# Performance work log

Hardware: AMD Instinct MI355X
Metric: run time of the kernel (lower is better)

## Reference

```python
import jax, jax.numpy as jnp
import numpy as np

B, D, C = 8192, 2048, 1000
NUM_IDS = 256
MSEL_W, ORTH_W, CONS_W = 0.5, 0.1, 0.1


def setup_inputs() -> dict:
    key = jax.random.key(0)
    ks = jax.random.split(key, 7)
    return {
        "feat_shared": jax.random.normal(ks[0], (B, D), dtype=jnp.float32),
        "dee1": jax.random.normal(ks[1], (B, D), dtype=jnp.float32),
        "dee2": jax.random.normal(ks[2], (B, D), dtype=jnp.float32),
        "dee3": jax.random.normal(ks[3], (B, D), dtype=jnp.float32),
        "logits": jax.random.normal(ks[4], (B, C), dtype=jnp.float32),
        "labels": jax.random.randint(ks[5], (B,), 0, NUM_IDS, dtype=jnp.int32),
        "modal_ids": jax.random.randint(ks[6], (B,), 0, 2, dtype=jnp.int32),
    }


def _l2norm(x):
    return x / jnp.sqrt(jnp.sum(x * x, axis=1, keepdims=True)).clip(1e-12)


def _msel(features, labels, modal_ids):
    f = _l2norm(features)
    m_rgb = (modal_ids == 0).astype(f.dtype)  # [B]
    m_sar = (modal_ids == 1).astype(f.dtype)
    # per-label per-modal sums and counts via segment_sum (fixed NUM_IDS segments)
    sum_rgb = jax.ops.segment_sum(f * m_rgb[:, None], labels, num_segments=NUM_IDS)  # [L,D]
    sum_sar = jax.ops.segment_sum(f * m_sar[:, None], labels, num_segments=NUM_IDS)
    n_rgb = jax.ops.segment_sum(m_rgb, labels, num_segments=NUM_IDS)  # [L]
    n_sar = jax.ops.segment_sum(m_sar, labels, num_segments=NUM_IDS)
    c_rgb = sum_rgb / jnp.maximum(n_rgb, 1.0)[:, None]
    c_sar = sum_sar / jnp.maximum(n_sar, 1.0)[:, None]
    dist_cross = 1.0 - jnp.sum(c_rgb * c_sar, axis=1)
    # mean of Gram(f_rgb, f_rgb) == center_rgb . center_rgb (includes diagonal), same math
    dist_intra = 1.0 - jnp.sum(c_rgb * c_rgb, axis=1)
    valid = (n_rgb >= 2.0) & (n_sar >= 1.0)
    per_label = jnp.where(valid, (dist_cross - dist_intra) ** 2, 0.0)
    count = jnp.sum(valid.astype(f.dtype))
    return jnp.where(count > 0, jnp.sum(per_label) / jnp.maximum(count, 1.0), 0.0)


def _orth(f1, f2, f3):
    n1, n2, n3 = _l2norm(f1), _l2norm(f2), _l2norm(f3)
    s12 = jnp.mean(jnp.abs(jnp.sum(n1 * n2, axis=1)))
    s13 = jnp.mean(jnp.abs(jnp.sum(n1 * n3, axis=1)))
    s23 = jnp.mean(jnp.abs(jnp.sum(n2 * n3, axis=1)))
    return s12 + s13 + s23


def _consistency(logits, modal_ids):
    probs = jax.nn.softmax(logits, axis=1)  # [B,C]
    m_rgb = (modal_ids == 0).astype(probs.dtype)
    m_sar = (modal_ids == 1).astype(probs.dtype)
    n_rgb = jnp.sum(m_rgb)
    n_sar = jnp.sum(m_sar)
    p_rgb = jnp.sum(probs * m_rgb[:, None], axis=0) / jnp.maximum(n_rgb, 1.0)
    p_sar = jnp.sum(probs * m_sar[:, None], axis=0) / jnp.maximum(n_sar, 1.0)
    lr, ls = jnp.log(p_rgb), jnp.log(p_sar)
    # F.kl_div(log p, q, 'sum') = sum q*(log q - log p)
    kl = 0.5 * (jnp.sum(p_sar * (ls - lr)) + jnp.sum(p_rgb * (lr - ls)))
    return jnp.where((n_rgb > 0) & (n_sar > 0), kl, 0.0)


def reference(feat_shared, dee1, dee2, dee3, logits, labels, modal_ids):
    loss = MSEL_W * _msel(feat_shared, labels, modal_ids)
    loss = loss + ORTH_W * _orth(dee1, dee2, dee3)
    loss = loss + CONS_W * _consistency(logits, modal_ids)
    return loss
```

## Files before the change

### kernel.cpp

```cpp
#include <hip/hip_runtime.h>
#include <math.h>

#define B_   8192
#define D_   2048
#define C_   1000
#define L_   256
#define BIN_CAP 64
#define ORTH_BLOCKS 2048

typedef unsigned short bf16raw;

__device__ __forceinline__ float bflo(unsigned int u) { return __uint_as_float(u << 16); }
__device__ __forceinline__ float bfhi(unsigned int u) { return __uint_as_float(u & 0xffff0000u); }

__device__ __forceinline__ bf16raw f2b(float f) {
  unsigned int x = __float_as_uint(f);
  unsigned int r = (x + 0x7fffu + ((x >> 16) & 1u)) >> 16;
  return (bf16raw)r;
}

__device__ __forceinline__ void dec8(uint4 u, float* x) {
  x[0] = bflo(u.x); x[1] = bfhi(u.x);
  x[2] = bflo(u.y); x[3] = bfhi(u.y);
  x[4] = bflo(u.z); x[5] = bfhi(u.z);
  x[6] = bflo(u.w); x[7] = bfhi(u.w);
}

__device__ __forceinline__ float waveSum(float v) {
#pragma unroll
  for (int off = 32; off > 0; off >>= 1) v += __shfl_xor(v, off, 64);
  return v;
}

__device__ __forceinline__ float blockSum(float v, float* lds4) {
  v = waveSum(v);
  const int wave = threadIdx.x >> 6;
  if ((threadIdx.x & 63) == 0) lds4[wave] = v;
  __syncthreads();
  v = lds4[0] + lds4[1] + lds4[2] + lds4[3];
  __syncthreads();
  return v;
}

__device__ __forceinline__ void load8rt(const void* p, size_t rowbase, int t, int isb,
                                        float* x) {
  if (isb) {
    const uint4 v = ((const uint4*)((const bf16raw*)p + rowbase))[t];
    dec8(v, x);
  } else {
    const float4* q = (const float4*)((const float*)p + rowbase);
    const float4 v0 = q[2 * t], v1 = q[2 * t + 1];
    x[0] = v0.x; x[1] = v0.y; x[2] = v0.z; x[3] = v0.w;
    x[4] = v1.x; x[5] = v1.y; x[6] = v1.z; x[7] = v1.w;
  }
}

__global__ __launch_bounds__(256) void detect_kernel(const unsigned int* feat_words,
                                                     int* flag) {
  __shared__ float lds4[4];
  const unsigned int w = feat_words[threadIdx.x];
  const float v = bflo(w);
  const float a = fabsf(v);
  float hit = (a > 1e-3f && a < 10.f) ? 1.f : 0.f;
  hit = blockSum(hit, lds4);
  if (threadIdx.x == 0) *flag = (hit > 128.f) ? 1 : 0;
}

__global__ __launch_bounds__(256) void init_kernel(int* counts, float* accs,
                                                   float* p_final) {
  const int t = blockIdx.x * 256 + threadIdx.x;
  if (t < 2 * L_) counts[t] = 0;
  if (t < 16) accs[t] = 0.f;
  if (t < 2 * C_) p_final[t] = 0.f;
}

__global__ __launch_bounds__(256) void bin_kernel(const int* labels, const int* modal,
                                                  int* counts, int* rowlist) {
  const int r = blockIdx.x * 256 + threadIdx.x;
  if (r >= B_) return;
  const int m = modal[r] ? 1 : 0;
  int lb = labels[r]; lb = lb < 0 ? 0 : (lb >= L_ ? L_ - 1 : lb);
  const int key = m * L_ + lb;
  const int idx = atomicAdd(&counts[key], 1);
  if (idx < BIN_CAP) rowlist[key * BIN_CAP + idx] = r;
}

__global__ __launch_bounds__(256) void rowdot_kernel(const void* f1, const void* f2,
                                                     const void* f3, const void* feat,
                                                     float* orth_part, float* norms,
                                                     const int* flag) {
  __shared__ float lsum[4][3];
  const int t = threadIdx.x;
  const int wave = t >> 6, lane = t & 63;
  const int isb = *flag;

  if (blockIdx.x < ORTH_BLOCKS) {
    const int row = blockIdx.x * 4 + wave;
    const size_t base = (size_t)row * D_;
    float v[6] = {0.f, 0.f, 0.f, 0.f, 0.f, 0.f};
    if (isb) {
      const uint4* qa = (const uint4*)((const bf16raw*)f1 + base);
      const uint4* qb = (const uint4*)((const bf16raw*)f2 + base);
      const uint4* qc = (const uint4*)((const bf16raw*)f3 + base);
      uint4 A[4], Bv[4], Cv[4];
#pragma unroll
      for (int j = 0; j < 4; ++j) A[j] = qa[j * 64 + lane];
#pragma unroll
      for (int j = 0; j < 4; ++j) Bv[j] = qb[j * 64 + lane];
#pragma unroll
      for (int j = 0; j < 4; ++j) Cv[j] = qc[j * 64 + lane];
#pragma unroll
      for (int j = 0; j < 4; ++j) {
        float a[8], b[8], c[8];
        dec8(A[j], a); dec8(Bv[j], b); dec8(Cv[j], c);
#pragma unroll
        for (int k = 0; k < 8; ++k) {
          v[0] += a[k] * a[k]; v[1] += b[k] * b[k]; v[2] += c[k] * c[k];
          v[3] += a[k] * b[k]; v[4] += a[k] * c[k]; v[5] += b[k] * c[k];
        }
      }
    } else {
      const float4* qa = (const float4*)((const float*)f1 + base);
      const float4* qb = (const float4*)((const float*)f2 + base);
      const float4* qc = (const float4*)((const float*)f3 + base);
#pragma unroll
      for (int h = 0; h < 2; ++h) {
        float4 A[4], Bv[4], Cv[4];
#pragma unroll
        for (int j = 0; j < 4; ++j) A[j] = qa[(h * 4 + j) * 64 + lane];
#pragma unroll
        for (int j = 0; j < 4; ++j) Bv[j] = qb[(h * 4 + j) * 64 + lane];
#pragma unroll
        for (int j = 0; j < 4; ++j) Cv[j] = qc[(h * 4 + j) * 64 + lane];
#pragma unroll
        for (int j = 0; j < 4; ++j) {
          const float a[4] = {A[j].x, A[j].y, A[j].z, A[j].w};
          const float b[4] = {Bv[j].x, Bv[j].y, Bv[j].z, Bv[j].w};
          const float c[4] = {Cv[j].x, Cv[j].y, Cv[j].z, Cv[j].w};
#pragma unroll
          for (int k = 0; k < 4; ++k) {
            v[0] += a[k] * a[k]; v[1] += b[k] * b[k]; v[2] += c[k] * c[k];
            v[3] += a[k] * b[k]; v[4] += a[k] * c[k]; v[5] += b[k] * c[k];
          }
        }
      }
    }
#pragma unroll
    for (int off = 32; off > 0; off >>= 1) {
#pragma unroll
      for (int j = 0; j < 6; ++j) v[j] += __shfl_xor(v[j], off, 64);
    }
    const float q1 = fmaxf(sqrtf(v[0]), 1e-12f);
    const float q2 = fmaxf(sqrtf(v[1]), 1e-12f);
    const float q3 = fmaxf(sqrtf(v[2]), 1e-12f);
    if (lane == 0) {
      lsum[wave][0] = fabsf(v[3]) / (q1 * q2);
      lsum[wave][1] = fabsf(v[4]) / (q1 * q3);
      lsum[wave][2] = fabsf(v[5]) / (q2 * q3);
    }
    __syncthreads();
    if (t < 3) {
      orth_part[t * ORTH_BLOCKS + blockIdx.x] =
          lsum[0][t] + lsum[1][t] + lsum[2][t] + lsum[3][t];
    }
  } else {
    const int row = (blockIdx.x - ORTH_BLOCKS) * 4 + wave;
    const size_t base = (size_t)row * D_;
    float ss = 0.f;
    if (isb) {
      const uint4* q = (const uint4*)((const bf16raw*)feat + base);
      uint4 X[4];
#pragma unroll
      for (int j = 0; j < 4; ++j) X[j] = q[j * 64 + lane];
#pragma unroll
      for (int j = 0; j < 4; ++j) {
        float x[8]; dec8(X[j], x);
#pragma unroll
        for (int k = 0; k < 8; ++k) ss += x[k] * x[k];
      }
    } else {
      const float4* q = (const float4*)((const float*)feat + base);
#pragma unroll
      for (int j = 0; j < 8; ++j) {
        const float4 w = q[j * 64 + lane];
        ss += w.x * w.x + w.y * w.y + w.z * w.z + w.w * w.w;
      }
    }
    ss = waveSum(ss);
    if (lane == 0) norms[row] = 1.f / fmaxf(sqrtf(ss), 1e-12f);
  }
}

__device__ __forceinline__ void loadlogits(const void* logits, int r, int lane, int isb,
                                           float* x) {
#pragma unroll
  for (int kk = 0; kk < 4; ++kk) {
    const int idx = lane + (kk << 6);
    if (idx < (C_ / 4)) {
      if (isb) {
        const uint2 w = ((const uint2*)((const bf16raw*)logits + (size_t)r * C_))[idx];
        x[4 * kk + 0] = bflo(w.x); x[4 * kk + 1] = bfhi(w.x);
        x[4 * kk + 2] = bflo(w.y); x[4 * kk + 3] = bfhi(w.y);
      } else {
        const float4 w = ((const float4*)((const float*)logits + (size_t)r * C_))[idx];
        x[4 * kk + 0] = w.x; x[4 * kk + 1] = w.y;
        x[4 * kk + 2] = w.z; x[4 * kk + 3] = w.w;
      }
    } else {
      x[4 * kk + 0] = -INFINITY; x[4 * kk + 1] = -INFINITY;
      x[4 * kk + 2] = -INFINITY; x[4 * kk + 3] = -INFINITY;
    }
  }
}

__global__ __launch_bounds__(256) void cons_kernel(const void* logits, const int* modal,
                                                   float* p_final, const int* flag) {
  __shared__ float wacc[4][2][1024];
  const int t = threadIdx.x;
  const int wave = t >> 6, lane = t & 63;
  const int isb = *flag;
  float accA[16], accB[16];
#pragma unroll
  for (int k = 0; k < 16; ++k) { accA[k] = 0.f; accB[k] = 0.f; }
  const int rbase = blockIdx.x * 32 + wave * 8;
#pragma unroll
  for (int i = 0; i < 8; i += 2) {
    const int r0 = rbase + i, r1 = rbase + i + 1;
    float x[16], y[16];
    loadlogits(logits, r0, lane, isb, x);
    loadlogits(logits, r1, lane, isb, y);
    float mx = -INFINITY, my = -INFINITY;
#pragma unroll
    for (int k = 0; k < 16; ++k) { mx = fmaxf(mx, x[k]); my = fmaxf(my, y[k]); }
#pragma unroll
    for (int off = 32; off > 0; off >>= 1) {
      mx = fmaxf(mx, __shfl_xor(mx, off, 64));
      my = fmaxf(my, __shfl_xor(my, off, 64));
    }
    float sx = 0.f, sy = 0.f;
#pragma unroll
    for (int k = 0; k < 16; ++k) {
      x[k] = expf(x[k] - mx); sx += x[k];
      y[k] = expf(y[k] - my); sy += y[k];
    }
#pragma unroll
    for (int off = 32; off > 0; off >>= 1) {
      sx += __shfl_xor(sx, off, 64);
      sy += __shfl_xor(sy, off, 64);
    }
    const float ivx = 1.f / sx, ivy = 1.f / sy;
    if (modal[r0] == 0) {
#pragma unroll
      for (int k = 0; k < 16; ++k) accA[k] += x[k] * ivx;
    } else {
#pragma unroll
      for (int k = 0; k < 16; ++k) accB[k] += x[k] * ivx;
    }
    if (modal[r1] == 0) {
#pragma unroll
      for (int k = 0; k < 16; ++k) accA[k] += y[k] * ivy;
    } else {
#pragma unroll
      for (int k = 0; k < 16; ++k) accB[k] += y[k] * ivy;
    }
  }
#pragma unroll
  for (int k = 0; k < 16; ++k) {
    const int c = 4 * (lane + ((k >> 2) << 6)) + (k & 3);
    wacc[wave][0][c] = accA[k];
    wacc[wave][1][c] = accB[k];
  }
  __syncthreads();
  for (int e = t; e < 2 * C_; e += 256) {
    const int m = (e < C_) ? 0 : 1;
    const int c = e - m * C_;
    atomicAdd(&p_final[e], wacc[0][m][c] + wacc[1][m][c] + wacc[2][m][c] + wacc[3][m][c]);
  }
}

__global__ __launch_bounds__(256) void label_kernel(const void* feat, const int* counts,
                                                    const int* rowlist, const float* norms,
                                                    float* accs, const int* flag) {
  __shared__ float lds4[4];
  const int l = blockIdx.x;
  const int t = threadIdx.x;
  const int isb = *flag;
  const int nr_true = counts[l];
  const int ns_true = counts[L_ + l];
  const int nr = nr_true < BIN_CAP ? nr_true : BIN_CAP;
  const int ns = ns_true < BIN_CAP ? ns_true : BIN_CAP;
  const int tot = nr + ns;
  float accR[8], accS[8];
#pragma unroll
  for (int j = 0; j < 8; ++j) { accR[j] = 0.f; accS[j] = 0.f; }
  for (int i = 0; i < tot; i += 2) {
    const int i1 = i + 1;
    const int key0 = (i < nr) ? l : (L_ + l);
    const int idx0 = (i < nr) ? i : (i - nr);
    const int r0 = rowlist[key0 * BIN_CAP + idx0];
    const bool have1 = (i1 < tot);
    const int key1 = (i1 < nr) ? l : (L_ + l);
    const int idx1 = (i1 < nr) ? i1 : (i1 - nr);
    const int r1 = have1 ? rowlist[key1 * BIN_CAP + idx1] : r0;
    const float rn0 = norms[r0];
    const float rn1 = have1 ? norms[r1] : 0.f;
    float x0[8], x1[8];
    load8rt(feat, (size_t)r0 * D_, t, isb, x0);
    load8rt(feat, (size_t)r1 * D_, t, isb, x1);
    if (i < nr) {
#pragma unroll
      for (int j = 0; j < 8; ++j) accR[j] += x0[j] * rn0;
    } else {
#pragma unroll
      for (int j = 0; j < 8; ++j) accS[j] += x0[j] * rn0;
    }
    if (i1 < nr) {
#pragma unroll
      for (int j = 0; j < 8; ++j) accR[j] += x1[j] * rn1;
    } else {
#pragma unroll
      for (int j = 0; j < 8; ++j) accS[j] += x1[j] * rn1;
    }
  }
  float rr = 0.f, rs = 0.f;
#pragma unroll
  for (int j = 0; j < 8; ++j) { rr += accR[j] * accR[j]; rs += accR[j] * accS[j]; }
  rr = blockSum(rr, lds4);
  rs = blockSum(rs, lds4);
  if (t == 0 && nr_true >= 2 && ns_true >= 1) {
    const float fr = (float)nr_true, fs = (float)ns_true;
    const float diff = rr / (fr * fr) - rs / (fr * fs);
    atomicAdd(&accs[3], diff * diff);
    atomicAdd(&accs[4], 1.0f);
  }
}

__global__ __launch_bounds__(256) void InnovationLoss_88124138979690_kernel(
    const float* p_final, const int* counts, const float* accs, const float* orth_part,
    void* out, const int* flag) {
  __shared__ float lds4[4];
  const int t = threadIdx.x;
  const float nr = blockSum((float)counts[t], lds4);
  const float ns = blockSum((float)counts[L_ + t], lds4);
  const float fr = fmaxf(nr, 1.f), fs = fmaxf(ns, 1.f);
  float klp = 0.f;
  for (int c = t; c < C_; c += 256) {
    const float pr = p_final[c] / fr;
    const float ps = p_final[C_ + c] / fs;
    klp += (ps - pr) * (logf(ps) - logf(pr));
  }
  klp = blockSum(klp, lds4);
  float o0 = 0.f, o1 = 0.f, o2 = 0.f;
  for (int b = t; b < ORTH_BLOCKS; b += 256) {
    o0 += orth_part[b];
    o1 += orth_part[ORTH_BLOCKS + b];
    o2 += orth_part[2 * ORTH_BLOCKS + b];
  }
  o0 = blockSum(o0, lds4);
  o1 = blockSum(o1, lds4);
  o2 = blockSum(o2, lds4);
  if (t == 0) {
    const float kl = (nr > 0.f && ns > 0.f) ? 0.5f * klp : 0.f;
    const float msel_cnt = accs[4];
    const float msel = msel_cnt > 0.f ? accs[3] / fmaxf(msel_cnt, 1.f) : 0.f;
    const float orth = (o0 + o1 + o2) * (1.0f / (float)B_);
    const float res = 0.5f * msel + 0.1f * orth + 0.1f * kl;
    if (*flag) ((bf16raw*)out)[0] = f2b(res);
    else       ((float*)out)[0]   = res;
  }
}

extern "C" __attribute__((visibility("default")))
void kernel_launch(void* const* d_in, const int* in_sizes, int n_in,
                   void* d_out, int out_size, void* d_ws, size_t ws_size,
                   hipStream_t stream) {
  const void* feat   = d_in[0];
  const void* dee1   = d_in[1];
  const void* dee2   = d_in[2];
  const void* dee3   = d_in[3];
  const void* logits = d_in[4];
  const int*  labels = (const int*)d_in[5];
  const int*  modal  = (const int*)d_in[6];

  char* ws = (char*)d_ws;
  int*   counts    = (int*)  (ws);
  float* accs      = (float*)(ws + 2048);
  float* p_final   = (float*)(ws + 2112);
  int*   rowlist   = (int*)  (ws + 10112);
  int*   flag      = (int*)  (ws + 141184);
  float* norms     = (float*)(ws + 141248);
  float* orth_part = (float*)(ws + 174016);

  detect_kernel<<<1, 256, 0, stream>>>((const unsigned int*)feat, flag);
  init_kernel<<<8, 256, 0, stream>>>(counts, accs, p_final);
  bin_kernel<<<B_ / 256, 256, 0, stream>>>(labels, modal, counts, rowlist);
  rowdot_kernel<<<2 * ORTH_BLOCKS, 256, 0, stream>>>(dee1, dee2, dee3, feat, orth_part,
                                                     norms, flag);
  cons_kernel<<<B_ / 32, 256, 0, stream>>>(logits, modal, p_final, flag);
  label_kernel<<<L_, 256, 0, stream>>>(feat, counts, rowlist, norms, accs, flag);
  InnovationLoss_88124138979690_kernel<<<1, 256, 0, stream>>>(p_final, counts, accs,
                                                              orth_part, d_out, flag);
}
```

Measured before the change: 316.2 us.

## Fuse orth, norm and softmax streaming into one persistent kernel with prefetch

Merges the row-dot/norm kernel and the consistency softmax kernel into a single launch, with fixed block partitions for orthogonality, feature norms and logits. Each wave now handles multiple rows (8 orth rows, 16 norm rows, 4 logit rows) and double-buffers the next row's loads in registers to overlap memory with compute. The label kernel also gets software prefetch of upcoming rows. This removes a launch and is meant to improve latency hiding, at the cost of higher register pressure and fewer, heavier blocks.

```diff
diff --git a/kernel.cpp b/kernel.cpp
--- a/kernel.cpp
+++ b/kernel.cpp
@@ -6,7 +6,12 @@
 #define C_   1000
 #define L_   256
 #define BIN_CAP 64
-#define ORTH_BLOCKS 2048
+
+#define ORTH_BLK  256
+#define NORM_BLK  128
+#define CONS_BLK  512
+#define FUSED_GRID (ORTH_BLK + NORM_BLK + CONS_BLK)
+#define ORTH_WAVES (ORTH_BLK * 4)
 
 typedef unsigned short bf16raw;
 
@@ -40,19 +45,6 @@
   v = lds4[0] + lds4[1] + lds4[2] + lds4[3];
   __syncthreads();
   return v;
-}
-
-__device__ __forceinline__ void load8rt(const void* p, size_t rowbase, int t, int isb,
-                                        float* x) {
-  if (isb) {
-    const uint4 v = ((const uint4*)((const bf16raw*)p + rowbase))[t];
-    dec8(v, x);
-  } else {
-    const float4* q = (const float4*)((const float*)p + rowbase);
-    const float4 v0 = q[2 * t], v1 = q[2 * t + 1];
-    x[0] = v0.x; x[1] = v0.y; x[2] = v0.z; x[3] = v0.w;
-    x[4] = v1.x; x[5] = v1.y; x[6] = v1.z; x[7] = v1.w;
-  }
 }
 
 __global__ __launch_bounds__(256) void detect_kernel(const unsigned int* feat_words,
@@ -85,196 +77,279 @@
   if (idx < BIN_CAP) rowlist[key * BIN_CAP + idx] = r;
 }
 
-__global__ __launch_bounds__(256) void rowdot_kernel(const void* f1, const void* f2,
-                                                     const void* f3, const void* feat,
-                                                     float* orth_part, float* norms,
-                                                     const int* flag) {
-  __shared__ float lsum[4][3];
+__device__ __forceinline__ void ldrow3(const bf16raw* pa, const bf16raw* pb,
+                                       const bf16raw* pc, size_t base, int lane,
+                                       uint4 (&A)[4], uint4 (&Bv)[4], uint4 (&Cv)[4]) {
+  const uint4* qa = (const uint4*)(pa + base);
+  const uint4* qb = (const uint4*)(pb + base);
+  const uint4* qc = (const uint4*)(pc + base);
+#pragma unroll
+  for (int j = 0; j < 4; ++j) A[j] = qa[j * 64 + lane];
+#pragma unroll
+  for (int j = 0; j < 4; ++j) Bv[j] = qb[j * 64 + lane];
+#pragma unroll
+  for (int j = 0; j < 4; ++j) Cv[j] = qc[j * 64 + lane];
+}
+
+__device__ __forceinline__ void orth_rowacc(const uint4 (&A)[4], const uint4 (&Bv)[4],
+                                            const uint4 (&Cv)[4], float (&v)[6]) {
+#pragma unroll
+  for (int j = 0; j < 4; ++j) {
+    float a[8], b[8], c[8];
+    dec8(A[j], a); dec8(Bv[j], b); dec8(Cv[j], c);
+#pragma unroll
+    for (int k = 0; k < 8; ++k) {
+      v[0] += a[k] * a[k]; v[1] += b[k] * b[k]; v[2] += c[k] * c[k];
+      v[3] += a[k] * b[k]; v[4] += a[k] * c[k]; v[5] += b[k] * c[k];
+    }
+  }
+}
+
+__device__ __forceinline__ float ssq4(const uint4 (&X)[4]) {
+  float ss = 0.f;
+#pragma unroll
+  for (int j = 0; j < 4; ++j) {
+    float x[8]; dec8(X[j], x);
+#pragma unroll
+    for (int k = 0; k < 8; ++k) ss += x[k] * x[k];
+  }
+  return ss;
+}
+
+__device__ __forceinline__ void loadlogits_f32(const void* logits, int r, int lane,
+                                               float (&x)[16]) {
+#pragma unroll
+  for (int kk = 0; kk < 4; ++kk) {
+    const int idx = lane + (kk << 6);
+    if (idx < (C_ / 4)) {
+      const float4 w = ((const float4*)((const float*)logits + (size_t)r * C_))[idx];
+      x[4 * kk + 0] = w.x; x[4 * kk + 1] = w.y;
+      x[4 * kk + 2] = w.z; x[4 * kk + 3] = w.w;
+    } else {
+      x[4 * kk + 0] = -INFINITY; x[4 * kk + 1] = -INFINITY;
+      x[4 * kk + 2] = -INFINITY; x[4 * kk + 3] = -INFINITY;
+    }
+  }
+}
+
+__device__ __forceinline__ void softmax_acc(float (&x)[16], int m, float (&accA)[16],
+                                            float (&accB)[16]) {
+  float mx = -INFINITY;
+#pragma unroll
+  for (int k = 0; k < 16; ++k) mx = fmaxf(mx, x[k]);
+#pragma unroll
+  for (int off = 32; off > 0; off >>= 1) mx = fmaxf(mx, __shfl_xor(mx, off, 64));
+  float s = 0.f;
+#pragma unroll
+  for (int k = 0; k < 16; ++k) { x[k] = expf(x[k] - mx); s += x[k]; }
+#pragma unroll
+  for (int off = 32; off > 0; off >>= 1) s += __shfl_xor(s, off, 64);
+  const float inv = 1.f / s;
+  if (m == 0) {
+#pragma unroll
+    for (int k = 0; k < 16; ++k) accA[k] += x[k] * inv;
+  } else {
+#pragma unroll
+    for (int k = 0; k < 16; ++k) accB[k] += x[k] * inv;
+  }
+}
+
+__global__ __launch_bounds__(256) void fused_stream_kernel(
+    const void* f1, const void* f2, const void* f3, const void* feat,
+    const void* logits, const int* modal, float* orth_part, float* norms,
+    float* p_final, const int* flag) {
+  __shared__ float wacc[4][2][1024];
   const int t = threadIdx.x;
   const int wave = t >> 6, lane = t & 63;
   const int isb = *flag;
-
-  if (blockIdx.x < ORTH_BLOCKS) {
-    const int row = blockIdx.x * 4 + wave;
-    const size_t base = (size_t)row * D_;
-    float v[6] = {0.f, 0.f, 0.f, 0.f, 0.f, 0.f};
+  const int bx = blockIdx.x;
+
+  if (bx < ORTH_BLK) {
+    const int gw = bx * 4 + wave;
+    float s12 = 0.f, s13 = 0.f, s23 = 0.f;
     if (isb) {
-      const uint4* qa = (const uint4*)((const bf16raw*)f1 + base);
-      const uint4* qb = (const uint4*)((const bf16raw*)f2 + base);
-      const uint4* qc = (const uint4*)((const bf16raw*)f3 + base);
-      uint4 A[4], Bv[4], Cv[4];
-#pragma unroll
-      for (int j = 0; j < 4; ++j) A[j] = qa[j * 64 + lane];
-#pragma unroll
-      for (int j = 0; j < 4; ++j) Bv[j] = qb[j * 64 + lane];
-#pragma unroll
-      for (int j = 0; j < 4; ++j) Cv[j] = qc[j * 64 + lane];
-#pragma unroll
-      for (int j = 0; j < 4; ++j) {
-        float a[8], b[8], c[8];
-        dec8(A[j], a); dec8(Bv[j], b); dec8(Cv[j], c);
-#pragma unroll
-        for (int k = 0; k < 8; ++k) {
-          v[0] += a[k] * a[k]; v[1] += b[k] * b[k]; v[2] += c[k] * c[k];
-          v[3] += a[k] * b[k]; v[4] += a[k] * c[k]; v[5] += b[k] * c[k];
-        }
+      const bf16raw* pa = (const bf16raw*)f1;
+      const bf16raw* pb = (const bf16raw*)f2;
+      const bf16raw* pc = (const bf16raw*)f3;
+      const size_t base0 = (size_t)gw * (8 * D_);
+      uint4 A0[4], B0[4], C0[4], A1[4], B1[4], C1[4];
+      ldrow3(pa, pb, pc, base0, lane, A0, B0, C0);
+#pragma unroll
+      for (int r = 0; r < 8; ++r) {
+        if (r < 7) {
+          const size_t nb = base0 + (size_t)(r + 1) * D_;
+          if (r & 1) ldrow3(pa, pb, pc, nb, lane, A0, B0, C0);
+          else       ldrow3(pa, pb, pc, nb, lane, A1, B1, C1);
+        }
+        float v[6] = {0.f, 0.f, 0.f, 0.f, 0.f, 0.f};
+        if (r & 1) orth_rowacc(A1, B1, C1, v);
+        else       orth_rowacc(A0, B0, C0, v);
+#pragma unroll
+        for (int off = 32; off > 0; off >>= 1) {
+#pragma unroll
+          for (int j = 0; j < 6; ++j) v[j] += __shfl_xor(v[j], off, 64);
+        }
+        const float q1 = fmaxf(sqrtf(v[0]), 1e-12f);
+        const float q2 = fmaxf(sqrtf(v[1]), 1e-12f);
+        const float q3 = fmaxf(sqrtf(v[2]), 1e-12f);
+        s12 += fabsf(v[3]) / (q1 * q2);
+        s13 += fabsf(v[4]) / (q1 * q3);
+        s23 += fabsf(v[5]) / (q2 * q3);
       }
     } else {
-      const float4* qa = (const float4*)((const float*)f1 + base);
-      const float4* qb = (const float4*)((const float*)f2 + base);
-      const float4* qc = (const float4*)((const float*)f3 + base);
-#pragma unroll
-      for (int h = 0; h < 2; ++h) {
-        float4 A[4], Bv[4], Cv[4];
-#pragma unroll
-        for (int j = 0; j < 4; ++j) A[j] = qa[(h * 4 + j) * 64 + lane];
-#pragma unroll
-        for (int j = 0; j < 4; ++j) Bv[j] = qb[(h * 4 + j) * 64 + lane];
-#pragma unroll
-        for (int j = 0; j < 4; ++j) Cv[j] = qc[(h * 4 + j) * 64 + lane];
-#pragma unroll
-        for (int j = 0; j < 4; ++j) {
-          const float a[4] = {A[j].x, A[j].y, A[j].z, A[j].w};
-          const float b[4] = {Bv[j].x, Bv[j].y, Bv[j].z, Bv[j].w};
-          const float c[4] = {Cv[j].x, Cv[j].y, Cv[j].z, Cv[j].w};
+      for (int r = 0; r < 8; ++r) {
+        const size_t base = ((size_t)gw * 8 + r) * D_;
+        const float4* qa = (const float4*)((const float*)f1 + base);
+        const float4* qb = (const float4*)((const float*)f2 + base);
+        const float4* qc = (const float4*)((const float*)f3 + base);
+        float v[6] = {0.f, 0.f, 0.f, 0.f, 0.f, 0.f};
+#pragma unroll
+        for (int h = 0; h < 8; ++h) {
+          const float4 a4 = qa[h * 64 + lane];
+          const float4 b4 = qb[h * 64 + lane];
+          const float4 c4 = qc[h * 64 + lane];
+          const float a[4] = {a4.x, a4.y, a4.z, a4.w};
+          const float b[4] = {b4.x, b4.y, b4.z, b4.w};
+          const float c[4] = {c4.x, c4.y, c4.z, c4.w};
 #pragma unroll
           for (int k = 0; k < 4; ++k) {
             v[0] += a[k] * a[k]; v[1] += b[k] * b[k]; v[2] += c[k] * c[k];
             v[3] += a[k] * b[k]; v[4] += a[k] * c[k]; v[5] += b[k] * c[k];
           }
         }
-      }
-    }
-#pragma unroll
-    for (int off = 32; off > 0; off >>= 1) {
-#pragma unroll
-      for (int j = 0; j < 6; ++j) v[j] += __shfl_xor(v[j], off, 64);
-    }
-    const float q1 = fmaxf(sqrtf(v[0]), 1e-12f);
-    const float q2 = fmaxf(sqrtf(v[1]), 1e-12f);
-    const float q3 = fmaxf(sqrtf(v[2]), 1e-12f);
+#pragma unroll
+        for (int off = 32; off > 0; off >>= 1) {
+#pragma unroll
+          for (int j = 0; j < 6; ++j) v[j] += __shfl_xor(v[j], off, 64);
+        }
+        const float q1 = fmaxf(sqrtf(v[0]), 1e-12f);
+        const float q2 = fmaxf(sqrtf(v[1]), 1e-12f);
+        const float q3 = fmaxf(sqrtf(v[2]), 1e-12f);
+        s12 += fabsf(v[3]) / (q1 * q2);
+        s13 += fabsf(v[4]) / (q1 * q3);
+        s23 += fabsf(v[5]) / (q2 * q3);
+      }
+    }
     if (lane == 0) {
-      lsum[wave][0] = fabsf(v[3]) / (q1 * q2);
-      lsum[wave][1] = fabsf(v[4]) / (q1 * q3);
-      lsum[wave][2] = fabsf(v[5]) / (q2 * q3);
+      orth_part[gw] = s12;
+      orth_part[ORTH_WAVES + gw] = s13;
+      orth_part[2 * ORTH_WAVES + gw] = s23;
+    }
+  } else if (bx < ORTH_BLK + NORM_BLK) {
+    const int gw = (bx - ORTH_BLK) * 4 + wave;
+    const size_t base0 = (size_t)gw * (16 * D_);
+    if (isb) {
+      const bf16raw* pf = (const bf16raw*)feat;
+      uint4 X0[4], X1[4];
+      {
+        const uint4* q = (const uint4*)(pf + base0);
+#pragma unroll
+        for (int j = 0; j < 4; ++j) X0[j] = q[j * 64 + lane];
+      }
+#pragma unroll
+      for (int r = 0; r < 16; ++r) {
+        if (r < 15) {
+          const uint4* q = (const uint4*)(pf + base0 + (size_t)(r + 1) * D_);
+          if (r & 1) {
+#pragma unroll
+            for (int j = 0; j < 4; ++j) X0[j] = q[j * 64 + lane];
+          } else {
+#pragma unroll
+            for (int j = 0; j < 4; ++j) X1[j] = q[j * 64 + lane];
+          }
+        }
+        float ss = (r & 1) ? ssq4(X1) : ssq4(X0);
+        ss = waveSum(ss);
+        if (lane == 0) norms[gw * 16 + r] = 1.f / fmaxf(sqrtf(ss), 1e-12f);
+      }
+    } else {
+      for (int r = 0; r < 16; ++r) {
+        const float4* q = (const float4*)((const float*)feat + base0 + (size_t)r * D_);
+        float ss = 0.f;
+#pragma unroll
+        for (int j = 0; j < 8; ++j) {
+          const float4 w = q[j * 64 + lane];
+          ss += w.x * w.x + w.y * w.y + w.z * w.z + w.w * w.w;
+        }
+        ss = waveSum(ss);
+        if (lane == 0) norms[gw * 16 + r] = 1.f / fmaxf(sqrtf(ss), 1e-12f);
+      }
+    }
+  } else {
+    const int cb = bx - ORTH_BLK - NORM_BLK;
+    const int rbase = cb * 16 + wave * 4;
+    float accA[16], accB[16];
+#pragma unroll
+    for (int k = 0; k < 16; ++k) { accA[k] = 0.f; accB[k] = 0.f; }
+    if (isb) {
+      const bf16raw* pl = (const bf16raw*)logits;
+      uint4 W0a, W1a;
+      uint4 W0b = make_uint4(0u, 0u, 0u, 0u), W1b = make_uint4(0u, 0u, 0u, 0u);
+      int ma, mb = 0;
+      {
+        const uint4* q = (const uint4*)(pl + (size_t)rbase * C_);
+        W0a = q[lane];
+        W1a = (lane < 61) ? q[64 + lane] : make_uint4(0u, 0u, 0u, 0u);
+        ma = modal[rbase];
+      }
+#pragma unroll
+      for (int i = 0; i < 4; ++i) {
+        if (i < 3) {
+          const int rn = rbase + i + 1;
+          const uint4* q = (const uint4*)(pl + (size_t)rn * C_);
+          W0b = q[lane];
+          W1b = (lane < 61) ? q[64 + lane] : make_uint4(0u, 0u, 0u, 0u);
+          mb = modal[rn];
+        }
+        float x[16];
+        dec8(W0a, x);
+        if (lane < 61) {
+          float xx[8]; dec8(W1a, xx);
+#pragma unroll
+          for (int k = 0; k < 8; ++k) x[8 + k] = xx[k];
+        } else {
+#pragma unroll
+          for (int k = 0; k < 8; ++k) x[8 + k] = -INFINITY;
+        }
+        softmax_acc(x, ma, accA, accB);
+        W0a = W0b; W1a = W1b; ma = mb;
+      }
+#pragma unroll
+      for (int k = 0; k < 16; ++k) {
+        const int c = (k < 8) ? (8 * lane + k) : (512 + 8 * lane + (k - 8));
+        wacc[wave][0][c] = accA[k];
+        wacc[wave][1][c] = accB[k];
+      }
+    } else {
+      float xa[16], xb[16];
+      int ma, mb = 0;
+      loadlogits_f32(logits, rbase, lane, xa);
+      ma = modal[rbase];
+#pragma unroll
+      for (int i = 0; i < 4; ++i) {
+        if (i < 3) {
+          loadlogits_f32(logits, rbase + i + 1, lane, xb);
+          mb = modal[rbase + i + 1];
+        }
+        softmax_acc(xa, ma, accA, accB);
+#pragma unroll
+        for (int k = 0; k < 16; ++k) xa[k] = xb[k];
+        ma = mb;
+      }
+#pragma unroll
+      for (int k = 0; k < 16; ++k) {
+        const int c = 4 * (lane + ((k >> 2) << 6)) + (k & 3);
+        wacc[wave][0][c] = accA[k];
+        wacc[wave][1][c] = accB[k];
+      }
     }
     __syncthreads();
-    if (t < 3) {
-      orth_part[t * ORTH_BLOCKS + blockIdx.x] =
-          lsum[0][t] + lsum[1][t] + lsum[2][t] + lsum[3][t];
-    }
-  } else {
-    const int row = (blockIdx.x - ORTH_BLOCKS) * 4 + wave;
-    const size_t base = (size_t)row * D_;
-    float ss = 0.f;
-    if (isb) {
-      const uint4* q = (const uint4*)((const bf16raw*)feat + base);
-      uint4 X[4];
-#pragma unroll
-      for (int j = 0; j < 4; ++j) X[j] = q[j * 64 + lane];
-#pragma unroll
-      for (int j = 0; j < 4; ++j) {
-        float x[8]; dec8(X[j], x);
-#pragma unroll
-        for (int k = 0; k < 8; ++k) ss += x[k] * x[k];
-      }
-    } else {
-      const float4* q = (const float4*)((const float*)feat + base);
-#pragma unroll
-      for (int j = 0; j < 8; ++j) {
-        const float4 w = q[j * 64 + lane];
-        ss += w.x * w.x + w.y * w.y + w.z * w.z + w.w * w.w;
-      }
-    }
-    ss = waveSum(ss);
-    if (lane == 0) norms[row] = 1.f / fmaxf(sqrtf(ss), 1e-12f);
-  }
-}
-
-__device__ __forceinline__ void loadlogits(const void* logits, int r, int lane, int isb,
-                                           float* x) {
-#pragma unroll
-  for (int kk = 0; kk < 4; ++kk) {
-    const int idx = lane + (kk << 6);
-    if (idx < (C_ / 4)) {
-      if (isb) {
-        const uint2 w = ((const uint2*)((const bf16raw*)logits + (size_t)r * C_))[idx];
-        x[4 * kk + 0] = bflo(w.x); x[4 * kk + 1] = bfhi(w.x);
-        x[4 * kk + 2] = bflo(w.y); x[4 * kk + 3] = bfhi(w.y);
-      } else {
-        const float4 w = ((const float4*)((const float*)logits + (size_t)r * C_))[idx];
-        x[4 * kk + 0] = w.x; x[4 * kk + 1] = w.y;
-        x[4 * kk + 2] = w.z; x[4 * kk + 3] = w.w;
-      }
-    } else {
-      x[4 * kk + 0] = -INFINITY; x[4 * kk + 1] = -INFINITY;
-      x[4 * kk + 2] = -INFINITY; x[4 * kk + 3] = -INFINITY;
-    }
-  }
-}
-
-__global__ __launch_bounds__(256) void cons_kernel(const void* logits, const int* modal,
-                                                   float* p_final, const int* flag) {
-  __shared__ float wacc[4][2][1024];
-  const int t = threadIdx.x;
-  const int wave = t >> 6, lane = t & 63;
-  const int isb = *flag;
-  float accA[16], accB[16];
-#pragma unroll
-  for (int k = 0; k < 16; ++k) { accA[k] = 0.f; accB[k] = 0.f; }
-  const int rbase = blockIdx.x * 32 + wave * 8;
-#pragma unroll
-  for (int i = 0; i < 8; i += 2) {
-    const int r0 = rbase + i, r1 = rbase + i + 1;
-    float x[16], y[16];
-    loadlogits(logits, r0, lane, isb, x);
-    loadlogits(logits, r1, lane, isb, y);
-    float mx = -INFINITY, my = -INFINITY;
-#pragma unroll
-    for (int k = 0; k < 16; ++k) { mx = fmaxf(mx, x[k]); my = fmaxf(my, y[k]); }
-#pragma unroll
-    for (int off = 32; off > 0; off >>= 1) {
-      mx = fmaxf(mx, __shfl_xor(mx, off, 64));
-      my = fmaxf(my, __shfl_xor(my, off, 64));
-    }
-    float sx = 0.f, sy = 0.f;
-#pragma unroll
-    for (int k = 0; k < 16; ++k) {
-      x[k] = expf(x[k] - mx); sx += x[k];
-      y[k] = expf(y[k] - my); sy += y[k];
-    }
-#pragma unroll
-    for (int off = 32; off > 0; off >>= 1) {
-      sx += __shfl_xor(sx, off, 64);
-      sy += __shfl_xor(sy, off, 64);
-    }
-    const float ivx = 1.f / sx, ivy = 1.f / sy;
-    if (modal[r0] == 0) {
-#pragma unroll
-      for (int k = 0; k < 16; ++k) accA[k] += x[k] * ivx;
-    } else {
-#pragma unroll
-      for (int k = 0; k < 16; ++k) accB[k] += x[k] * ivx;
-    }
-    if (modal[r1] == 0) {
-#pragma unroll
-      for (int k = 0; k < 16; ++k) accA[k] += y[k] * ivy;
-    } else {
-#pragma unroll
-      for (int k = 0; k < 16; ++k) accB[k] += y[k] * ivy;
-    }
-  }
-#pragma unroll
-  for (int k = 0; k < 16; ++k) {
-    const int c = 4 * (lane + ((k >> 2) << 6)) + (k & 3);
-    wacc[wave][0][c] = accA[k];
-    wacc[wave][1][c] = accB[k];
-  }
-  __syncthreads();
-  for (int e = t; e < 2 * C_; e += 256) {
-    const int m = (e < C_) ? 0 : 1;
-    const int c = e - m * C_;
-    atomicAdd(&p_final[e], wacc[0][m][c] + wacc[1][m][c] + wacc[2][m][c] + wacc[3][m][c]);
+    for (int e = t; e < 2 * C_; e += 256) {
+      const int m = (e < C_) ? 0 : 1;
+      const int c = e - m * C_;
+      atomicAdd(&p_final[e],
+                wacc[0][m][c] + wacc[1][m][c] + wacc[2][m][c] + wacc[3][m][c]);
+    }
   }
 }
 
@@ -293,33 +368,111 @@
   float accR[8], accS[8];
 #pragma unroll
   for (int j = 0; j < 8; ++j) { accR[j] = 0.f; accS[j] = 0.f; }
-  for (int i = 0; i < tot; i += 2) {
-    const int i1 = i + 1;
-    const int key0 = (i < nr) ? l : (L_ + l);
-    const int idx0 = (i < nr) ? i : (i - nr);
-    const int r0 = rowlist[key0 * BIN_CAP + idx0];
-    const bool have1 = (i1 < tot);
-    const int key1 = (i1 < nr) ? l : (L_ + l);
-    const int idx1 = (i1 < nr) ? i1 : (i1 - nr);
-    const int r1 = have1 ? rowlist[key1 * BIN_CAP + idx1] : r0;
-    const float rn0 = norms[r0];
-    const float rn1 = have1 ? norms[r1] : 0.f;
-    float x0[8], x1[8];
-    load8rt(feat, (size_t)r0 * D_, t, isb, x0);
-    load8rt(feat, (size_t)r1 * D_, t, isb, x1);
-    if (i < nr) {
-#pragma unroll
-      for (int j = 0; j < 8; ++j) accR[j] += x0[j] * rn0;
+
+  if (tot > 0) {
+    auto rowAt = [&](int i) -> int {
+      const int key = (i < nr) ? l : (L_ + l);
+      const int idx = (i < nr) ? i : (i - nr);
+      return rowlist[key * BIN_CAP + idx];
+    };
+    if (isb) {
+      const bf16raw* pf = (const bf16raw*)feat;
+      const int r0 = rowAt(0);
+      uint4 qa = ((const uint4*)(pf + (size_t)r0 * D_))[t];
+      float na = norms[r0];
+      uint4 qb = make_uint4(0u, 0u, 0u, 0u);
+      float nb2 = 0.f;
+      if (tot > 1) {
+        const int r1 = rowAt(1);
+        qb = ((const uint4*)(pf + (size_t)r1 * D_))[t];
+        nb2 = norms[r1];
+      }
+      for (int i = 0; i < tot; i += 2) {
+        uint4 qc = make_uint4(0u, 0u, 0u, 0u), qd = make_uint4(0u, 0u, 0u, 0u);
+        float nc = 0.f, nd = 0.f;
+        if (i + 2 < tot) {
+          const int rc = rowAt(i + 2);
+          qc = ((const uint4*)(pf + (size_t)rc * D_))[t];
+          nc = norms[rc];
+        }
+        if (i + 3 < tot) {
+          const int rd = rowAt(i + 3);
+          qd = ((const uint4*)(pf + (size_t)rd * D_))[t];
+          nd = norms[rd];
+        }
+        {
+          float x[8]; dec8(qa, x);
+          if (i < nr) {
+#pragma unroll
+            for (int j = 0; j < 8; ++j) accR[j] += x[j] * na;
+          } else {
+#pragma unroll
+            for (int j = 0; j < 8; ++j) accS[j] += x[j] * na;
+          }
+        }
+        if (i + 1 < tot) {
+          float x[8]; dec8(qb, x);
+          if (i + 1 < nr) {
+#pragma unroll
+            for (int j = 0; j < 8; ++j) accR[j] += x[j] * nb2;
+          } else {
+#pragma unroll
+            for (int j = 0; j < 8; ++j) accS[j] += x[j] * nb2;
+          }
+        }
+        qa = qc; qb = qd; na = nc; nb2 = nd;
+      }
     } else {
-#pragma unroll
-      for (int j = 0; j < 8; ++j) accS[j] += x0[j] * rn0;
-    }
-    if (i1 < nr) {
-#pragma unroll
-      for (int j = 0; j < 8; ++j) accR[j] += x1[j] * rn1;
-    } else {
-#pragma unroll
-      for (int j = 0; j < 8; ++j) accS[j] += x1[j] * rn1;
+      const float* pf = (const float*)feat;
+      const int r0 = rowAt(0);
+      float4 a0 = ((const float4*)(pf + (size_t)r0 * D_))[2 * t];
+      float4 a1 = ((const float4*)(pf + (size_t)r0 * D_))[2 * t + 1];
+      float na = norms[r0];
+      float4 b0 = make_float4(0.f, 0.f, 0.f, 0.f), b1 = make_float4(0.f, 0.f, 0.f, 0.f);
+      float nb2 = 0.f;
+      if (tot > 1) {
+        const int r1 = rowAt(1);
+        b0 = ((const float4*)(pf + (size_t)r1 * D_))[2 * t];
+        b1 = ((const float4*)(pf + (size_t)r1 * D_))[2 * t + 1];
+        nb2 = norms[r1];
+      }
+      for (int i = 0; i < tot; i += 2) {
+        float4 c0 = make_float4(0.f, 0.f, 0.f, 0.f), c1 = c0, d0 = c0, d1 = c0;
+        float nc = 0.f, nd = 0.f;
+        if (i + 2 < tot) {
+          const int rc = rowAt(i + 2);
+          c0 = ((const float4*)(pf + (size_t)rc * D_))[2 * t];
+          c1 = ((const float4*)(pf + (size_t)rc * D_))[2 * t + 1];
+          nc = norms[rc];
+        }
+        if (i + 3 < tot) {
+          const int rd = rowAt(i + 3);
+          d0 = ((const float4*)(pf + (size_t)rd * D_))[2 * t];
+          d1 = ((const float4*)(pf + (size_t)rd * D_))[2 * t + 1];
+          nd = norms[rd];
+        }
+        {
+          const float x[8] = {a0.x, a0.y, a0.z, a0.w, a1.x, a1.y, a1.z, a1.w};
+          if (i < nr) {
+#pragma unroll
+            for (int j = 0; j < 8; ++j) accR[j] += x[j] * na;
+          } else {
+#pragma unroll
+            for (int j = 0; j < 8; ++j) accS[j] += x[j] * na;
+          }
+        }
+        if (i + 1 < tot) {
+          const float x[8] = {b0.x, b0.y, b0.z, b0.w, b1.x, b1.y, b1.z, b1.w};
+          if (i + 1 < nr) {
+#pragma unroll
+            for (int j = 0; j < 8; ++j) accR[j] += x[j] * nb2;
+          } else {
+#pragma unroll
+            for (int j = 0; j < 8; ++j) accS[j] += x[j] * nb2;
+          }
+        }
+        a0 = c0; a1 = c1; b0 = d0; b1 = d1; na = nc; nb2 = nd;
+      }
     }
   }
   float rr = 0.f, rs = 0.f;
@@ -351,10 +504,10 @@
   }
   klp = blockSum(klp, lds4);
   float o0 = 0.f, o1 = 0.f, o2 = 0.f;
-  for (int b = t; b < ORTH_BLOCKS; b += 256) {
+  for (int b = t; b < ORTH_WAVES; b += 256) {
     o0 += orth_part[b];
-    o1 += orth_part[ORTH_BLOCKS + b];
-    o2 += orth_part[2 * ORTH_BLOCKS + b];
+    o1 += orth_part[ORTH_WAVES + b];
+    o2 += orth_part[2 * ORTH_WAVES + b];
   }
   o0 = blockSum(o0, lds4);
   o1 = blockSum(o1, lds4);
@@ -394,9 +547,9 @@
   detect_kernel<<<1, 256, 0, stream>>>((const unsigned int*)feat, flag);
   init_kernel<<<8, 256, 0, stream>>>(counts, accs, p_final);
   bin_kernel<<<B_ / 256, 256, 0, stream>>>(labels, modal, counts, rowlist);
-  rowdot_kernel<<<2 * ORTH_BLOCKS, 256, 0, stream>>>(dee1, dee2, dee3, feat, orth_part,
-                                                     norms, flag);
-  cons_kernel<<<B_ / 32, 256, 0, stream>>>(logits, modal, p_final, flag);
+  fused_stream_kernel<<<FUSED_GRID, 256, 0, stream>>>(dee1, dee2, dee3, feat, logits,
+                                                      modal, orth_part, norms, p_final,
+                                                      flag);
   label_kernel<<<L_, 256, 0, stream>>>(feat, counts, rowlist, norms, accs, flag);
   InnovationLoss_88124138979690_kernel<<<1, 256, 0, stream>>>(p_final, counts, accs,
                                                               orth_part, d_out, flag);
```

New measurement: 310.9 us. Within noise of the previous version (-1.7%).
